# Performance work log

Hardware: AMD Instinct MI355X
Metric: run time of the kernel (lower is better)

Reference implementation:

```python
import jax, jax.numpy as jnp
import numpy as np

N = 100000      # nodes
E = 1600000     # edges (avg degree 16)
EMB = 128
L = 3           # num_layers
NUM_OPS = 64
MAX_BW = 64     # max_bitwidth
P = 4           # max_num_params


def setup_inputs() -> dict:
    key = jax.random.key(0)
    ks = jax.random.split(key, 24)
    w = lambda k, s: jax.random.normal(k, s, jnp.float32) * 0.05
    return {
        "ops": jax.random.randint(ks[0], (N,), 0, NUM_OPS),
        "params": jax.random.randint(ks[1], (N, P), 0, MAX_BW),
        "edge_src": jax.random.randint(ks[2], (E,), 0, N),
        "edge_dst": jax.random.randint(ks[3], (E,), 0, N),
        "op_emb_table": w(ks[4], (NUM_OPS, EMB)),
        "param_emb_table": w(ks[5], (MAX_BW, EMB)),
        "opmlp_w1": w(ks[6], ((1 + P) * EMB, EMB)), "opmlp_b1": w(ks[7], (EMB,)),
        "opmlp_w2": w(ks[8], (EMB, EMB)), "opmlp_b2": w(ks[9], (EMB,)),
        "conv_w": w(ks[10], (L, EMB, EMB)), "conv_b": w(ks[11], (L, EMB)),
        "mlp_w1": w(ks[12], (L * EMB, EMB)), "mlp_b1": w(ks[13], (EMB,)),
        "mlp_w2": w(ks[14], (EMB, EMB)), "mlp_b2": w(ks[15], (EMB,)),
        "mlpinv_w1": w(ks[16], (L * EMB, EMB)), "mlpinv_b1": w(ks[17], (EMB,)),
        "mlpinv_w2": w(ks[18], (EMB, EMB)), "mlpinv_b2": w(ks[19], (EMB,)),
        "comb_w": w(ks[20], (2 * EMB, EMB)), "comb_b": w(ks[21], (EMB,)),
    }


def _lrelu(x):
    return jax.nn.leaky_relu(x)  # slope 0.01, matches nn.LeakyReLU default


def _gin_mean(feat, src, dst, w, b):
    # DGL GINConv(aggregator='mean', eps=0): apply_func(feat + mean_in_neighbors(feat))
    n = feat.shape[0]
    msg = jax.ops.segment_sum(feat[src], dst, num_segments=n)           # [N, EMB]
    deg = jax.ops.segment_sum(jnp.ones(src.shape, feat.dtype), dst, num_segments=n)
    agg = msg / jnp.maximum(deg, 1.0)[:, None]
    return _lrelu((feat + agg) @ w + b)


def reference(ops, params, edge_src, edge_dst,
              op_emb_table, param_emb_table,
              opmlp_w1, opmlp_b1, opmlp_w2, opmlp_b2,
              conv_w, conv_b,
              mlp_w1, mlp_b1, mlp_w2, mlp_b2,
              mlpinv_w1, mlpinv_b1, mlpinv_w2, mlpinv_b2,
              comb_w, comb_b):
    n = ops.shape[0]
    # OpEmb: cat([op_emb] + per-param embs) -> MLP
    op_e = op_emb_table[ops]                               # [N, EMB]
    par_e = param_emb_table[params].reshape(n, -1)         # [N, P*EMB]
    h = jnp.concatenate([op_e, par_e], axis=1)
    h = _lrelu(h @ opmlp_w1 + opmlp_b1) @ opmlp_w2 + opmlp_b2
    states = h
    states_inv = h  # op_emb called twice on same inputs in the original

    conv_outs = []
    for i in range(L):
        states = _gin_mean(states, edge_src, edge_dst, conv_w[i], conv_b[i])
        conv_outs.append(states.sum(axis=0))
    final_sum = states.sum(axis=0)

    conv_outs_inv = []
    for i in range(L):
        states_inv = _gin_mean(states_inv, edge_dst, edge_src, conv_w[i], conv_b[i])
        # NOTE: original code appends states.sum(dim=0) (the final forward states),
        # not states_inv -- faithfully reproduced.
        conv_outs_inv.append(final_sum)

    g_emb = _lrelu(jnp.concatenate(conv_outs) @ mlp_w1 + mlp_b1) @ mlp_w2 + mlp_b2
    g_inv_emb = _lrelu(jnp.concatenate(conv_outs_inv) @ mlpinv_w1 + mlpinv_b1) @ mlpinv_w2 + mlpinv_b2

    out1 = jnp.concatenate([g_emb, g_inv_emb]) @ comb_w + comb_b          # [EMB]
    out2 = jnp.concatenate([states, states_inv], axis=1) @ comb_w + comb_b  # [N, EMB]
    return (out1, out2)
```

## Files before the change

### kernel.cpp

```cpp
#include <hip/hip_runtime.h>


typedef unsigned int  uint;
typedef unsigned short ushort;
typedef float  f32x4  __attribute__((ext_vector_type(4)));
typedef short  bf16x8 __attribute__((ext_vector_type(8)));

#define ABITS 9
#define CAPB  12288
#define CHUNK 2048

__device__ __forceinline__ float lrelu(float x) { return x > 0.0f ? x : 0.01f * x; }
__device__ __forceinline__ ushort f2b(float x) {
    uint u = __float_as_uint(x);
    return (ushort)((u + 0x7fffu + ((u >> 16) & 1u)) >> 16);
}
__device__ __forceinline__ float lof(uint u) { return __uint_as_float(u << 16); }
__device__ __forceinline__ float hif(uint u) { return __uint_as_float(u & 0xffff0000u); }

__global__ __launch_bounds__(256) void buildprep_kernel(
    const int* __restrict__ esrc, const int* __restrict__ edst, int E, int nb, int nChunks,
    int* __restrict__ gcur, uint2* __restrict__ binbuf,
    const float* __restrict__ opT, const float* __restrict__ parT,
    const float* __restrict__ W1, float* __restrict__ Atab,
    const float* __restrict__ convw, const float* __restrict__ ow2,
    const float* __restrict__ cw, ushort* __restrict__ Wt)
{
    __shared__ int hist[448];
    __shared__ int lstart[448];
    __shared__ int gbase[448];
    __shared__ int lcur[448];
    __shared__ int gsum[8];
    __shared__ uint sKey[CHUNK * 2];
    __shared__ uint sPay[CHUNK * 2];
    __shared__ ushort sBin[CHUNK * 2];
    int tid = threadIdx.x, lane = tid & 63;

    if ((int)blockIdx.x >= nChunks) {
        int rb = (int)blockIdx.x - nChunks;
        if (rb < 160) {
            int b = (rb << 1) | (tid >> 7);
            int t = b >> 6, v = b & 63, j = tid & 127;
            const float* emb = (t == 0 ? opT : parT) + v * 128;
            const float* w = W1 + (size_t)t * 128 * 128;
            float acc = 0.f;
            for (int k = 0; k < 128; ++k) acc += emb[k] * w[k * 128 + j];
            Atab[(size_t)b * 128 + j] = acc;
        } else {
            int t = (rb - 160) * 256 + tid;
            int img = t >> 14, idx = t & 16383;
            int k = idx >> 7, c = idx & 127;
            const float* src;
            if (img < 3)       src = convw + img * 16384;
            else if (img == 3) src = ow2;
            else               src = cw + (img - 4) * 16384;
            float v = src[k * 128 + c];
            int byteoff = (img << 15) + (c << 8) + ((((k >> 3) ^ (c & 7)) << 4)) + ((k & 7) << 1);
            Wt[byteoff >> 1] = f2b(v);
        }
        return;
    }

    int nb2 = nb * 2;
    int base = (int)blockIdx.x * CHUNK;
    int cnt = min(CHUNK, E - base);
    for (int i = tid; i < 448; i += 256) hist[i] = 0;
    __syncthreads();
    int s[8], d[8];
    #pragma unroll
    for (int i = 0; i < 8; ++i) {
        int idx = i * 256 + tid;
        if (idx < cnt) {
            s[i] = esrc[base + idx];
            d[i] = edst[base + idx];
            atomicAdd(&hist[d[i] >> ABITS], 1);
            atomicAdd(&hist[nb + (s[i] >> ABITS)], 1);
        } else s[i] = -1;
    }
    __syncthreads();
    #pragma unroll
    for (int k = 0; k < 2; ++k) {
        int idx = k * 256 + tid;
        int v = (idx < 448) ? hist[idx] : 0;
        int p = v;
        #pragma unroll
        for (int sh = 1; sh < 64; sh <<= 1) { int t = __shfl_up(p, sh, 64); if (lane >= sh) p += t; }
        if (idx < 448) {
            lstart[idx] = p - v;
            if (lane == 63) gsum[idx >> 6] = p;
        }
    }
    __syncthreads();
    if (tid == 0) { int run = 0; for (int g = 0; g < 7; ++g) { int t = gsum[g]; gsum[g] = run; run += t; } }
    __syncthreads();
    #pragma unroll
    for (int k = 0; k < 2; ++k) {
        int idx = k * 256 + tid;
        if (idx < 448) lstart[idx] += gsum[idx >> 6];
    }
    __syncthreads();
    for (int i = tid; i < nb2; i += 256) {
        int h = hist[i];
        gbase[i] = h ? atomicAdd(&gcur[i], h) : 0;
        lcur[i] = lstart[i];
    }
    __syncthreads();
    #pragma unroll
    for (int i = 0; i < 8; ++i) {
        if (s[i] >= 0) {
            int bf = d[i] >> ABITS;
            int p = atomicAdd(&lcur[bf], 1);
            sKey[p] = (uint)d[i]; sPay[p] = (uint)s[i]; sBin[p] = (ushort)bf;
            int bi = nb + (s[i] >> ABITS);
            int q = atomicAdd(&lcur[bi], 1);
            sKey[q] = (uint)s[i]; sPay[q] = (uint)d[i]; sBin[q] = (ushort)bi;
        }
    }
    __syncthreads();
    int total = 2 * cnt;
    for (int p = tid; p < total; p += 256) {
        int b = sBin[p];
        int pos = gbase[b] + (p - lstart[b]);
        if (pos < CAPB) binbuf[(size_t)b * CAPB + pos] = make_uint2(sKey[p], sPay[p]);
    }
}

__device__ __forceinline__ void stage_w(const ushort* __restrict__ img, ushort* ldsW, int tid)
{
    const uint4* s = (const uint4*)img;
    uint4* d = (uint4*)ldsW;
    #pragma unroll
    for (int i = 0; i < 4; ++i) d[tid + (i << 9)] = s[tid + (i << 9)];
}

__global__ __launch_bounds__(512, 2) void mid_kernel(
    const uint2* __restrict__ binbuf, const int* __restrict__ gcur, int nb, int N,
    int* __restrict__ csr_f, int* __restrict__ off_f, int* __restrict__ cnt_f,
    int* __restrict__ csr_i, int* __restrict__ off_i, int* __restrict__ cnt_i,
    const int* __restrict__ ops, const int* __restrict__ params,
    const float* __restrict__ Atab, const float* __restrict__ b1,
    const ushort* __restrict__ W2img, const float* __restrict__ b2,
    ushort* __restrict__ S0)
{
    __shared__ __align__(16) ushort ldsW[16384];
    __shared__ __align__(16) ushort ldsA[16384];
    int tid = threadIdx.x, lane = tid & 63, w = tid >> 6;
    int nb2 = 2 * nb;

    if ((int)blockIdx.x < nb2) {
        int* hist = (int*)ldsA;
        int* cur  = hist + 512;
        int* gsum = cur + 512;
        int b = blockIdx.x;
        int dir = (b >= nb) ? 1 : 0;
        int binLocal = dir ? b - nb : b;
        int node0 = binLocal << ABITS;
        int nn = min(512, N - node0);
        int total = min(gcur[b], CAPB);
        const uint2* seg = binbuf + (size_t)b * CAPB;
        int* csr = dir ? csr_i : csr_f;
        int* off = dir ? off_i : off_f;
        int* cnt = dir ? cnt_i : cnt_f;

        hist[tid] = 0;
        __syncthreads();
        for (int e = tid; e < total; e += 512) {
            uint2 kp = seg[e];
            atomicAdd(&hist[kp.x - (uint)node0], 1);
        }
        __syncthreads();
        int v = hist[tid];
        int p = v;
        #pragma unroll
        for (int sh = 1; sh < 64; sh <<= 1) { int t = __shfl_up(p, sh, 64); if (lane >= sh) p += t; }
        if (lane == 63) gsum[w] = p;
        __syncthreads();
        if (tid == 0) { int run = 0; for (int g = 0; g < 8; ++g) { int t = gsum[g]; gsum[g] = run; run += t; } }
        __syncthreads();
        int lv = p - v + gsum[w];
        cur[tid] = lv;
        int csrBase = binLocal * CAPB;
        if (tid < nn) { off[node0 + tid] = csrBase + lv; cnt[node0 + tid] = v; }
        __syncthreads();
        int* csrSeg = csr + csrBase;
        for (int e = tid; e < total; e += 512) {
            uint2 kp = seg[e];
            int q = atomicAdd(&cur[kp.x - (uint)node0], 1);
            csrSeg[q] = (int)(kp.y << 8);
        }
        return;
    }

    int node0 = ((int)blockIdx.x - nb2) << 7;
    stage_w(W2img, ldsW, tid);

    int r = tid >> 2, sub = tid & 3;
    int g = node0 + r;
    float4 acc4[8];
    if (g < N) {
        int op = ops[g];
        const float4* T = (const float4*)(Atab + ((size_t)op << 7) + (sub << 5));
        #pragma unroll
        for (int q = 0; q < 8; ++q) acc4[q] = T[q];
        #pragma unroll
        for (int p = 0; p < 4; ++p) {
            int pv = params[(g << 2) + p];
            const float4* Tp = (const float4*)(Atab + ((size_t)((p + 1) * 64 + pv) << 7) + (sub << 5));
            #pragma unroll
            for (int q = 0; q < 8; ++q) {
                float4 u = Tp[q];
                acc4[q].x += u.x; acc4[q].y += u.y; acc4[q].z += u.z; acc4[q].w += u.w;
            }
        }
        const float4* Bv = (const float4*)(b1 + (sub << 5));
        #pragma unroll
        for (int q = 0; q < 8; ++q) {
            float4 bb = Bv[q];
            acc4[q].x = lrelu(acc4[q].x + bb.x);
            acc4[q].y = lrelu(acc4[q].y + bb.y);
            acc4[q].z = lrelu(acc4[q].z + bb.z);
            acc4[q].w = lrelu(acc4[q].w + bb.w);
        }
    } else {
        #pragma unroll
        for (int q = 0; q < 8; ++q) acc4[q] = make_float4(0.f, 0.f, 0.f, 0.f);
    }
    int akey = r & 7;
    #pragma unroll
    for (int q2 = 0; q2 < 4; ++q2) {
        int ch = (sub << 2) + q2;
        float4 a = acc4[q2 * 2], b = acc4[q2 * 2 + 1];
        uint4 pk;
        pk.x = (uint)f2b(a.x) | ((uint)f2b(a.y) << 16);
        pk.y = (uint)f2b(a.z) | ((uint)f2b(a.w) << 16);
        pk.z = (uint)f2b(b.x) | ((uint)f2b(b.y) << 16);
        pk.w = (uint)f2b(b.z) | ((uint)f2b(b.w) << 16);
        *(uint4*)((char*)ldsA + r * 256 + ((ch ^ akey) << 4)) = pk;
    }
    __syncthreads();

    int l15 = lane & 15, lg = lane >> 4;
    int node = node0 + (w << 4) + l15;
    int brow = (w << 4) + l15;
    const char* Bb = (const char*)ldsA + brow * 256;
    int bkey = (brow & 7) << 4;
    f32x4 acc[8];
    #pragma unroll
    for (int i = 0; i < 8; ++i) acc[i] = f32x4{0.f, 0.f, 0.f, 0.f};
    #pragma unroll
    for (int kk = 0; kk < 4; ++kk) {
        bf16x8 bfr = *(const bf16x8*)(Bb + ((((kk << 2) + lg) << 4) ^ bkey));
        #pragma unroll
        for (int ct = 0; ct < 8; ++ct) {
            int c = (ct << 4) + l15;
            const char* Ab = (const char*)ldsW + c * 256;
            bf16x8 af = *(const bf16x8*)(Ab + ((((kk << 2) + lg) << 4) ^ ((c & 7) << 4)));
            acc[ct] = __builtin_amdgcn_mfma_f32_16x16x32_bf16(af, bfr, acc[ct], 0, 0, 0);
        }
    }
    if (node < N) {
        #pragma unroll
        for (int ct = 0; ct < 8; ++ct) {
            int ch0 = (ct << 4) + (lg << 2);
            float4 bb = *(const float4*)(b2 + ch0);
            uint2 pk;
            pk.x = (uint)f2b(acc[ct][0] + bb.x) | ((uint)f2b(acc[ct][1] + bb.y) << 16);
            pk.y = (uint)f2b(acc[ct][2] + bb.z) | ((uint)f2b(acc[ct][3] + bb.w) << 16);
            *(uint2*)((char*)S0 + ((size_t)node << 8) + (ch0 << 1)) = pk;
        }
    }
}

__global__ __launch_bounds__(256, 8) void agg2_kernel(
    const ushort* __restrict__ Sf, const ushort* __restrict__ Si,
    const int* __restrict__ csr_f, const int* __restrict__ off_f, const int* __restrict__ cnt_f,
    const int* __restrict__ csr_i, const int* __restrict__ off_i, const int* __restrict__ cnt_i,
    ushort* __restrict__ msgf, ushort* __restrict__ msgi, int N)
{
    int gw = (blockIdx.x * 256 + threadIdx.x) >> 6;
    int lane = threadIdx.x & 63;
    int dir = 0, g = gw;
    if (g >= N) { dir = 1; g -= N; if (g >= N) return; }
    const char* Sp = (const char*)(dir ? Si : Sf);
    const int* csr = dir ? csr_i : csr_f;
    int off = (dir ? off_i : off_f)[g];
    int deg = (dir ? cnt_i : cnt_f)[g];
    int half = lane >> 5;
    int lb = (lane & 31) << 3;

    float a0 = 0.f, a1 = 0.f, a2 = 0.f, a3 = 0.f;
    int d = 0;
    for (; d + 8 <= deg; d += 8) {
        int b0 = csr[off + d + 0 + half];
        int b1 = csr[off + d + 2 + half];
        int b2 = csr[off + d + 4 + half];
        int b3 = csr[off + d + 6 + half];
        uint2 v0 = *(const uint2*)(Sp + (uint)(b0 + lb));
        uint2 v1 = *(const uint2*)(Sp + (uint)(b1 + lb));
        uint2 v2 = *(const uint2*)(Sp + (uint)(b2 + lb));
        uint2 v3 = *(const uint2*)(Sp + (uint)(b3 + lb));
        a0 += (lof(v0.x) + lof(v1.x)) + (lof(v2.x) + lof(v3.x));
        a1 += (hif(v0.x) + hif(v1.x)) + (hif(v2.x) + hif(v3.x));
        a2 += (lof(v0.y) + lof(v1.y)) + (lof(v2.y) + lof(v3.y));
        a3 += (hif(v0.y) + hif(v1.y)) + (hif(v2.y) + hif(v3.y));
    }
    for (; d + 2 <= deg; d += 2) {
        int b = csr[off + d + half];
        uint2 v = *(const uint2*)(Sp + (uint)(b + lb));
        a0 += lof(v.x); a1 += hif(v.x); a2 += lof(v.y); a3 += hif(v.y);
    }
    if (d < deg && half == 0) {
        int b = csr[off + d];
        uint2 v = *(const uint2*)(Sp + (uint)(b + lb));
        a0 += lof(v.x); a1 += hif(v.x); a2 += lof(v.y); a3 += hif(v.y);
    }
    a0 += __shfl_xor(a0, 32);
    a1 += __shfl_xor(a1, 32);
    a2 += __shfl_xor(a2, 32);
    a3 += __shfl_xor(a3, 32);
    float invd = 1.0f / fmaxf((float)deg, 1.0f);
    uint2 self = *(const uint2*)(Sp + ((size_t)g << 8) + lb);
    a0 = lof(self.x) + a0 * invd;
    a1 = hif(self.x) + a1 * invd;
    a2 = lof(self.y) + a2 * invd;
    a3 = hif(self.y) + a3 * invd;
    if (half == 0) {
        uint2 pk;
        pk.x = (uint)f2b(a0) | ((uint)f2b(a1) << 16);
        pk.y = (uint)f2b(a2) | ((uint)f2b(a3) << 16);
        *(uint2*)((char*)(dir ? msgi : msgf) + ((size_t)g << 8) + lb) = pk;
    }
}

__global__ __launch_bounds__(512, 8) void gemm2_kernel(
    const ushort* __restrict__ msgf, const ushort* __restrict__ msgi,
    ushort* __restrict__ Sf_out, ushort* __restrict__ Si_out,
    const ushort* __restrict__ Wimg, const float* __restrict__ bias,
    float* __restrict__ colsum, int N)
{
    __shared__ __align__(16) ushort ldsW[16384];
    __shared__ float ldsCS[128];
    int tid = threadIdx.x, lane = tid & 63, w = tid >> 6;
    bool fwd = (blockIdx.x & 1) == 0;
    int node0 = (blockIdx.x >> 1) << 7;
    const ushort* msg = fwd ? msgf : msgi;
    ushort* Sout = fwd ? Sf_out : Si_out;

    stage_w(Wimg, ldsW, tid);
    if (fwd && tid < 128) ldsCS[tid] = 0.f;
    __syncthreads();

    int l15 = lane & 15, lg = lane >> 4;
    int node = node0 + (w << 4) + l15;
    int gr = min(node, N - 1);
    const char* Bb = (const char*)msg + ((size_t)gr << 8);

    f32x4 acc[8];
    #pragma unroll
    for (int i = 0; i < 8; ++i) acc[i] = f32x4{0.f, 0.f, 0.f, 0.f};
    #pragma unroll
    for (int kk = 0; kk < 4; ++kk) {
        bf16x8 bfr = *(const bf16x8*)(Bb + (((kk << 2) + lg) << 4));
        #pragma unroll
        for (int ct = 0; ct < 8; ++ct) {
            int c = (ct << 4) + l15;
            const char* Ab = (const char*)ldsW + c * 256;
            bf16x8 af = *(const bf16x8*)(Ab + ((((kk << 2) + lg) << 4) ^ ((c & 7) << 4)));
            acc[ct] = __builtin_amdgcn_mfma_f32_16x16x32_bf16(af, bfr, acc[ct], 0, 0, 0);
        }
    }

    bool valid = node < N;
    #pragma unroll
    for (int ct = 0; ct < 8; ++ct) {
        int ch0 = (ct << 4) + (lg << 2);
        float4 bb = *(const float4*)(bias + ch0);
        float o0 = lrelu(acc[ct][0] + bb.x);
        float o1 = lrelu(acc[ct][1] + bb.y);
        float o2 = lrelu(acc[ct][2] + bb.z);
        float o3 = lrelu(acc[ct][3] + bb.w);
        if (valid) {
            uint2 pk;
            pk.x = (uint)f2b(o0) | ((uint)f2b(o1) << 16);
            pk.y = (uint)f2b(o2) | ((uint)f2b(o3) << 16);
            *(uint2*)((char*)Sout + ((size_t)node << 8) + (ch0 << 1)) = pk;
        }
        if (fwd) {
            float c0 = valid ? o0 : 0.f, c1 = valid ? o1 : 0.f;
            float c2 = valid ? o2 : 0.f, c3 = valid ? o3 : 0.f;
            #pragma unroll
            for (int m = 1; m < 16; m <<= 1) {
                c0 += __shfl_xor(c0, m);
                c1 += __shfl_xor(c1, m);
                c2 += __shfl_xor(c2, m);
                c3 += __shfl_xor(c3, m);
            }
            if (l15 == 0) {
                atomicAdd(&ldsCS[ch0 + 0], c0);
                atomicAdd(&ldsCS[ch0 + 1], c1);
                atomicAdd(&ldsCS[ch0 + 2], c2);
                atomicAdd(&ldsCS[ch0 + 3], c3);
            }
        }
    }
    if (fwd) {
        __syncthreads();
        if (tid < 128) atomicAdd(&colsum[tid], ldsCS[tid]);
    }
}

__device__ __forceinline__ void final_body(
    float* lds, const float* __restrict__ convsum,
    const float* __restrict__ mw1, const float* __restrict__ mb1,
    const float* __restrict__ mw2, const float* __restrict__ mb2,
    const float* __restrict__ iw1, const float* __restrict__ ib1,
    const float* __restrict__ iw2, const float* __restrict__ ib2,
    const float* __restrict__ cw, const float* __restrict__ cb,
    float* __restrict__ out1)
{
    float* x  = lds;
    float* pa = lds + 384;
    float* pb = lds + 896;
    float* t1 = lds + 1408;
    float* t2 = lds + 1536;
    int tid = threadIdx.x, j = tid & 127, s = tid >> 7;
    if (tid < 384) x[tid] = convsum[tid];
    __syncthreads();
    float a = 0.f, c = 0.f;
    for (int k = s * 96; k < s * 96 + 96; ++k) {
        a += x[k] * mw1[k * 128 + j];
        c += x[256 + (k & 127)] * iw1[k * 128 + j];
    }
    pa[tid] = a; pb[tid] = c;
    __syncthreads();
    if (s == 0) {
        t1[j] = lrelu(pa[j] + pa[128 + j] + pa[256 + j] + pa[384 + j] + mb1[j]);
        t2[j] = lrelu(pb[j] + pb[128 + j] + pb[256 + j] + pb[384 + j] + ib1[j]);
    }
    __syncthreads();
    float b = 0.f, d = 0.f;
    for (int k = s * 32; k < s * 32 + 32; ++k) {
        b += t1[k] * mw2[k * 128 + j];
        d += t2[k] * iw2[k * 128 + j];
    }
    pa[tid] = b; pb[tid] = d;
    __syncthreads();
    if (s == 0) {
        t1[j] = pa[j] + pa[128 + j] + pa[256 + j] + pa[384 + j] + mb2[j];
        t2[j] = pb[j] + pb[128 + j] + pb[256 + j] + pb[384 + j] + ib2[j];
    }
    __syncthreads();
    float e = 0.f;
    for (int k = s * 32; k < s * 32 + 32; ++k)
        e += t1[k] * cw[k * 128 + j] + t2[k] * cw[(128 + k) * 128 + j];
    pa[tid] = e;
    __syncthreads();
    if (s == 0) out1[j] = pa[j] + pa[128 + j] + pa[256 + j] + pa[384 + j] + cb[j];
}

__global__ __launch_bounds__(512, 4) void out2_fused(
    const ushort* __restrict__ Sf, const ushort* __restrict__ Si,
    const ushort* __restrict__ CWimg, const float* __restrict__ cb,
    float* __restrict__ out, int gemmBlocks, int N,
    const float* __restrict__ convsum,
    const float* __restrict__ mw1, const float* __restrict__ mb1,
    const float* __restrict__ mw2, const float* __restrict__ mb2,
    const float* __restrict__ iw1, const float* __restrict__ ib1,
    const float* __restrict__ iw2, const float* __restrict__ ib2,
    const float* __restrict__ cw, float* __restrict__ out1)
{
    __shared__ __align__(16) ushort ldsW[16384];
    int tid = threadIdx.x, lane = tid & 63, w = tid >> 6;
    if ((int)blockIdx.x >= gemmBlocks) {
        final_body((float*)ldsW, convsum, mw1, mb1, mw2, mb2,
                   iw1, ib1, iw2, ib2, cw, cb, out1);
        return;
    }
    int node0 = blockIdx.x << 7;
    int l15 = lane & 15, lg = lane >> 4;
    int node = node0 + (w << 4) + l15;
    int gr = min(node, N - 1);
    f32x4 acc[8];
    #pragma unroll
    for (int i = 0; i < 8; ++i) acc[i] = f32x4{0.f, 0.f, 0.f, 0.f};
    #pragma unroll
    for (int pass = 0; pass < 2; ++pass) {
        if (pass) __syncthreads();
        stage_w(CWimg + (pass << 14), ldsW, tid);
        __syncthreads();
        const char* Bb = (const char*)(pass ? Si : Sf) + ((size_t)gr << 8);
        #pragma unroll
        for (int kk = 0; kk < 4; ++kk) {
            bf16x8 bfr = *(const bf16x8*)(Bb + (((kk << 2) + lg) << 4));
            #pragma unroll
            for (int ct = 0; ct < 8; ++ct) {
                int c = (ct << 4) + l15;
                const char* Ab = (const char*)ldsW + c * 256;
                bf16x8 af = *(const bf16x8*)(Ab + ((((kk << 2) + lg) << 4) ^ ((c & 7) << 4)));
                acc[ct] = __builtin_amdgcn_mfma_f32_16x16x32_bf16(af, bfr, acc[ct], 0, 0, 0);
            }
        }
    }
    if (node < N) {
        #pragma unroll
        for (int ct = 0; ct < 8; ++ct) {
            int ch0 = (ct << 4) + (lg << 2);
            float4 bb = *(const float4*)(cb + ch0);
            float4 o;
            o.x = acc[ct][0] + bb.x;
            o.y = acc[ct][1] + bb.y;
            o.z = acc[ct][2] + bb.z;
            o.w = acc[ct][3] + bb.w;
            *(float4*)(out + (size_t)node * 128 + ch0) = o;
        }
    }
}

extern "C" void kernel_launch(void* const* d_in, const int* in_sizes, int n_in,
                              void* d_out, int out_size, void* d_ws, size_t ws_size,
                              hipStream_t stream)
{
    (void)n_in; (void)out_size; (void)ws_size;
    const int*   ops    = (const int*)d_in[0];
    const int*   params = (const int*)d_in[1];
    const int*   esrc   = (const int*)d_in[2];
    const int*   edst   = (const int*)d_in[3];
    const float* opT    = (const float*)d_in[4];
    const float* parT   = (const float*)d_in[5];
    const float* ow1    = (const float*)d_in[6];
    const float* ob1    = (const float*)d_in[7];
    const float* ow2    = (const float*)d_in[8];
    const float* ob2    = (const float*)d_in[9];
    const float* convw  = (const float*)d_in[10];
    const float* convb  = (const float*)d_in[11];
    const float* mw1    = (const float*)d_in[12];
    const float* mb1    = (const float*)d_in[13];
    const float* mw2    = (const float*)d_in[14];
    const float* mb2    = (const float*)d_in[15];
    const float* iw1    = (const float*)d_in[16];
    const float* ib1    = (const float*)d_in[17];
    const float* iw2    = (const float*)d_in[18];
    const float* ib2    = (const float*)d_in[19];
    const float* cw     = (const float*)d_in[20];
    const float* cb     = (const float*)d_in[21];

    const int N = in_sizes[0];
    const int E = in_sizes[2];
    const int nb = (N + 511) >> ABITS;
    const size_t NP = (size_t)N * 128;

    ushort* S0   = (ushort*)d_ws;
    ushort* S1   = S0 + NP;
    ushort* S2   = S1 + NP;
    ushort* S3   = S2 + NP;
    ushort* Wt   = S3 + NP;
    float*  Atab = (float*)(Wt + 6 * 16384);
    float*  convsum = Atab + 320 * 128;
    int*    gcur = (int*)(convsum + 512);
    uint2*  binbuf = (uint2*)(gcur + 512);
    int*    csr_f = (int*)(binbuf + (size_t)2 * nb * CAPB);
    int*    csr_i = csr_f + (size_t)nb * CAPB;
    int*    off_f = csr_i + (size_t)nb * CAPB;
    int*    cnt_f = off_f + N;
    int*    off_i = cnt_f + N;
    int*    cnt_i = off_i + N;

    float* out1 = (float*)d_out;
    float* out2 = out1 + 128;
    ushort* MSGF = (ushort*)out2;
    ushort* MSGI = MSGF + NP;

    hipMemsetAsync(convsum, 0, sizeof(float) * 1024, stream);

    const int nChunks = (E + CHUNK - 1) / CHUNK;
    buildprep_kernel<<<nChunks + 160 + 384, 256, 0, stream>>>(
        esrc, edst, E, nb, nChunks, gcur, binbuf,
        opT, parT, ow1, Atab, convw, ow2, cw, Wt);

    const int grid = (N + 127) / 128;
    mid_kernel<<<2 * nb + grid, 512, 0, stream>>>(
        binbuf, gcur, nb, N,
        csr_f, off_f, cnt_f, csr_i, off_i, cnt_i,
        ops, params, Atab, ob1, Wt + 3 * 16384, ob2, S0);

    const int aggGrid = (2 * N + 3) / 4;
    agg2_kernel<<<aggGrid, 256, 0, stream>>>(S0, S0, csr_f, off_f, cnt_f, csr_i, off_i, cnt_i, MSGF, MSGI, N);
    gemm2_kernel<<<2 * grid, 512, 0, stream>>>(MSGF, MSGI, S1, S3, Wt,             convb,       convsum,       N);
    agg2_kernel<<<aggGrid, 256, 0, stream>>>(S1, S3, csr_f, off_f, cnt_f, csr_i, off_i, cnt_i, MSGF, MSGI, N);
    gemm2_kernel<<<2 * grid, 512, 0, stream>>>(MSGF, MSGI, S0, S2, Wt + 16384,     convb + 128, convsum + 128, N);
    agg2_kernel<<<aggGrid, 256, 0, stream>>>(S0, S2, csr_f, off_f, cnt_f, csr_i, off_i, cnt_i, MSGF, MSGI, N);
    gemm2_kernel<<<2 * grid, 512, 0, stream>>>(MSGF, MSGI, S1, S3, Wt + 2 * 16384, convb + 256, convsum + 256, N);

    out2_fused<<<grid + 1, 512, 0, stream>>>(S1, S3, Wt + 4 * 16384, cb, out2, grid, N,
                                             convsum, mw1, mb1, mw2, mb2,
                                             iw1, ib1, iw2, ib2, cw, out1);
}
```

Baseline: 655.3 us.

## Fuse GIN aggregation and layer GEMM into one kernel per layer

Merges the separate aggregation and GEMM kernels into one kernel per layer. Each 256-thread block gathers 16 nodes' mean-aggregated features into shared memory, then runs MFMA against weights read straight from global memory (no LDS staging). This drops the global round trip of the message buffers and three launches. Column-sum atomics are spread over 8 replicas, which the final kernel reduces. The cost is weight fragments fetched from global/L2 by every small block, and lower GEMM reuse per block.

```diff
diff --git a/kernel.cpp b/kernel.cpp
--- a/kernel.cpp
+++ b/kernel.cpp
@@ -271,141 +271,140 @@
     }
 }
 
-__global__ __launch_bounds__(256, 8) void agg2_kernel(
-    const ushort* __restrict__ Sf, const ushort* __restrict__ Si,
+__global__ __launch_bounds__(256, 8) void glayer_kernel(
+    const ushort* __restrict__ Sf_in, const ushort* __restrict__ Si_in,
+    ushort* __restrict__ Sf_out, ushort* __restrict__ Si_out,
     const int* __restrict__ csr_f, const int* __restrict__ off_f, const int* __restrict__ cnt_f,
     const int* __restrict__ csr_i, const int* __restrict__ off_i, const int* __restrict__ cnt_i,
-    ushort* __restrict__ msgf, ushort* __restrict__ msgi, int N)
+    const ushort* __restrict__ Wimg, const float* __restrict__ bias,
+    float* __restrict__ colsumR, int nBlkF, int N)
 {
-    int gw = (blockIdx.x * 256 + threadIdx.x) >> 6;
-    int lane = threadIdx.x & 63;
-    int dir = 0, g = gw;
-    if (g >= N) { dir = 1; g -= N; if (g >= N) return; }
-    const char* Sp = (const char*)(dir ? Si : Sf);
-    const int* csr = dir ? csr_i : csr_f;
-    int off = (dir ? off_i : off_f)[g];
-    int deg = (dir ? cnt_i : cnt_f)[g];
+    __shared__ __align__(16) char msgL[16 * 272];
+    __shared__ float ldsCS[128];
+    int tid = threadIdx.x, lane = tid & 63, w = tid >> 6;
+    bool fwd = (int)blockIdx.x < nBlkF;
+    int blkLocal = fwd ? (int)blockIdx.x : (int)blockIdx.x - nBlkF;
+    const char* Sp = (const char*)(fwd ? Sf_in : Si_in);
+    ushort* Sout = fwd ? Sf_out : Si_out;
+    const int* csr  = fwd ? csr_f : csr_i;
+    const int* offA = fwd ? off_f : off_i;
+    const int* cntA = fwd ? cnt_f : cnt_i;
+
+    if (tid < 128) ldsCS[tid] = 0.f;
+
     int half = lane >> 5;
     int lb = (lane & 31) << 3;
-
-    float a0 = 0.f, a1 = 0.f, a2 = 0.f, a3 = 0.f;
-    int d = 0;
-    for (; d + 8 <= deg; d += 8) {
-        int b0 = csr[off + d + 0 + half];
-        int b1 = csr[off + d + 2 + half];
-        int b2 = csr[off + d + 4 + half];
-        int b3 = csr[off + d + 6 + half];
-        uint2 v0 = *(const uint2*)(Sp + (uint)(b0 + lb));
-        uint2 v1 = *(const uint2*)(Sp + (uint)(b1 + lb));
-        uint2 v2 = *(const uint2*)(Sp + (uint)(b2 + lb));
-        uint2 v3 = *(const uint2*)(Sp + (uint)(b3 + lb));
-        a0 += (lof(v0.x) + lof(v1.x)) + (lof(v2.x) + lof(v3.x));
-        a1 += (hif(v0.x) + hif(v1.x)) + (hif(v2.x) + hif(v3.x));
-        a2 += (lof(v0.y) + lof(v1.y)) + (lof(v2.y) + lof(v3.y));
-        a3 += (hif(v0.y) + hif(v1.y)) + (hif(v2.y) + hif(v3.y));
-    }
-    for (; d + 2 <= deg; d += 2) {
-        int b = csr[off + d + half];
-        uint2 v = *(const uint2*)(Sp + (uint)(b + lb));
-        a0 += lof(v.x); a1 += hif(v.x); a2 += lof(v.y); a3 += hif(v.y);
-    }
-    if (d < deg && half == 0) {
-        int b = csr[off + d];
-        uint2 v = *(const uint2*)(Sp + (uint)(b + lb));
-        a0 += lof(v.x); a1 += hif(v.x); a2 += lof(v.y); a3 += hif(v.y);
-    }
-    a0 += __shfl_xor(a0, 32);
-    a1 += __shfl_xor(a1, 32);
-    a2 += __shfl_xor(a2, 32);
-    a3 += __shfl_xor(a3, 32);
-    float invd = 1.0f / fmaxf((float)deg, 1.0f);
-    uint2 self = *(const uint2*)(Sp + ((size_t)g << 8) + lb);
-    a0 = lof(self.x) + a0 * invd;
-    a1 = hif(self.x) + a1 * invd;
-    a2 = lof(self.y) + a2 * invd;
-    a3 = hif(self.y) + a3 * invd;
-    if (half == 0) {
-        uint2 pk;
-        pk.x = (uint)f2b(a0) | ((uint)f2b(a1) << 16);
-        pk.y = (uint)f2b(a2) | ((uint)f2b(a3) << 16);
-        *(uint2*)((char*)(dir ? msgi : msgf) + ((size_t)g << 8) + lb) = pk;
-    }
-}
-
-__global__ __launch_bounds__(512, 8) void gemm2_kernel(
-    const ushort* __restrict__ msgf, const ushort* __restrict__ msgi,
-    ushort* __restrict__ Sf_out, ushort* __restrict__ Si_out,
-    const ushort* __restrict__ Wimg, const float* __restrict__ bias,
-    float* __restrict__ colsum, int N)
-{
-    __shared__ __align__(16) ushort ldsW[16384];
-    __shared__ float ldsCS[128];
-    int tid = threadIdx.x, lane = tid & 63, w = tid >> 6;
-    bool fwd = (blockIdx.x & 1) == 0;
-    int node0 = (blockIdx.x >> 1) << 7;
-    const ushort* msg = fwd ? msgf : msgi;
-    ushort* Sout = fwd ? Sf_out : Si_out;
-
-    stage_w(Wimg, ldsW, tid);
-    if (fwd && tid < 128) ldsCS[tid] = 0.f;
+    int node0 = blkLocal << 4;
+
+    #pragma unroll
+    for (int i = 0; i < 4; ++i) {
+        int g = node0 + (w << 2) + i;
+        float a0 = 0.f, a1 = 0.f, a2 = 0.f, a3 = 0.f;
+        if (g < N) {
+            int off = offA[g], deg = cntA[g];
+            int d = 0;
+            for (; d + 8 <= deg; d += 8) {
+                int b0 = csr[off + d + 0 + half];
+                int b1 = csr[off + d + 2 + half];
+                int b2 = csr[off + d + 4 + half];
+                int b3 = csr[off + d + 6 + half];
+                uint2 v0 = *(const uint2*)(Sp + (uint)(b0 + lb));
+                uint2 v1 = *(const uint2*)(Sp + (uint)(b1 + lb));
+                uint2 v2 = *(const uint2*)(Sp + (uint)(b2 + lb));
+                uint2 v3 = *(const uint2*)(Sp + (uint)(b3 + lb));
+                a0 += (lof(v0.x) + lof(v1.x)) + (lof(v2.x) + lof(v3.x));
+                a1 += (hif(v0.x) + hif(v1.x)) + (hif(v2.x) + hif(v3.x));
+                a2 += (lof(v0.y) + lof(v1.y)) + (lof(v2.y) + lof(v3.y));
+                a3 += (hif(v0.y) + hif(v1.y)) + (hif(v2.y) + hif(v3.y));
+            }
+            for (; d + 2 <= deg; d += 2) {
+                int b = csr[off + d + half];
+                uint2 v = *(const uint2*)(Sp + (uint)(b + lb));
+                a0 += lof(v.x); a1 += hif(v.x); a2 += lof(v.y); a3 += hif(v.y);
+            }
+            if (d < deg && half == 0) {
+                int b = csr[off + d];
+                uint2 v = *(const uint2*)(Sp + (uint)(b + lb));
+                a0 += lof(v.x); a1 += hif(v.x); a2 += lof(v.y); a3 += hif(v.y);
+            }
+            a0 += __shfl_xor(a0, 32);
+            a1 += __shfl_xor(a1, 32);
+            a2 += __shfl_xor(a2, 32);
+            a3 += __shfl_xor(a3, 32);
+            float iv = 1.0f / fmaxf((float)deg, 1.0f);
+            uint2 self = *(const uint2*)(Sp + ((size_t)g << 8) + lb);
+            a0 = lof(self.x) + a0 * iv;
+            a1 = hif(self.x) + a1 * iv;
+            a2 = lof(self.y) + a2 * iv;
+            a3 = hif(self.y) + a3 * iv;
+        }
+        if (half == 0) {
+            uint2 pk;
+            pk.x = (uint)f2b(a0) | ((uint)f2b(a1) << 16);
+            pk.y = (uint)f2b(a2) | ((uint)f2b(a3) << 16);
+            *(uint2*)(msgL + ((w << 2) + i) * 272 + lb) = pk;
+        }
+    }
     __syncthreads();
 
     int l15 = lane & 15, lg = lane >> 4;
-    int node = node0 + (w << 4) + l15;
-    int gr = min(node, N - 1);
-    const char* Bb = (const char*)msg + ((size_t)gr << 8);
-
-    f32x4 acc[8];
-    #pragma unroll
-    for (int i = 0; i < 8; ++i) acc[i] = f32x4{0.f, 0.f, 0.f, 0.f};
+    const char* Bb = msgL + l15 * 272;
+    f32x4 acc0 = f32x4{0.f, 0.f, 0.f, 0.f};
+    f32x4 acc1 = f32x4{0.f, 0.f, 0.f, 0.f};
+    int ct0 = w << 1;
+    int c0 = (ct0 << 4) + l15;
+    int c1 = ((ct0 + 1) << 4) + l15;
+    const char* A0 = (const char*)Wimg + c0 * 256;
+    const char* A1 = (const char*)Wimg + c1 * 256;
+    int k0 = (c0 & 7) << 4, k1 = (c1 & 7) << 4;
     #pragma unroll
     for (int kk = 0; kk < 4; ++kk) {
-        bf16x8 bfr = *(const bf16x8*)(Bb + (((kk << 2) + lg) << 4));
-        #pragma unroll
-        for (int ct = 0; ct < 8; ++ct) {
-            int c = (ct << 4) + l15;
-            const char* Ab = (const char*)ldsW + c * 256;
-            bf16x8 af = *(const bf16x8*)(Ab + ((((kk << 2) + lg) << 4) ^ ((c & 7) << 4)));
-            acc[ct] = __builtin_amdgcn_mfma_f32_16x16x32_bf16(af, bfr, acc[ct], 0, 0, 0);
-        }
-    }
-
-    bool valid = node < N;
-    #pragma unroll
-    for (int ct = 0; ct < 8; ++ct) {
-        int ch0 = (ct << 4) + (lg << 2);
+        int chk = ((kk << 2) + lg) << 4;
+        bf16x8 bfr = *(const bf16x8*)(Bb + chk);
+        bf16x8 af0 = *(const bf16x8*)(A0 + (chk ^ k0));
+        bf16x8 af1 = *(const bf16x8*)(A1 + (chk ^ k1));
+        acc0 = __builtin_amdgcn_mfma_f32_16x16x32_bf16(af0, bfr, acc0, 0, 0, 0);
+        acc1 = __builtin_amdgcn_mfma_f32_16x16x32_bf16(af1, bfr, acc1, 0, 0, 0);
+    }
+
+    int gs = node0 + l15;
+    bool valid = gs < N;
+    #pragma unroll
+    for (int q = 0; q < 2; ++q) {
+        f32x4 a = q ? acc1 : acc0;
+        int ch0 = ((ct0 + q) << 4) + (lg << 2);
         float4 bb = *(const float4*)(bias + ch0);
-        float o0 = lrelu(acc[ct][0] + bb.x);
-        float o1 = lrelu(acc[ct][1] + bb.y);
-        float o2 = lrelu(acc[ct][2] + bb.z);
-        float o3 = lrelu(acc[ct][3] + bb.w);
+        float o0 = lrelu(a[0] + bb.x);
+        float o1 = lrelu(a[1] + bb.y);
+        float o2 = lrelu(a[2] + bb.z);
+        float o3 = lrelu(a[3] + bb.w);
         if (valid) {
             uint2 pk;
             pk.x = (uint)f2b(o0) | ((uint)f2b(o1) << 16);
             pk.y = (uint)f2b(o2) | ((uint)f2b(o3) << 16);
-            *(uint2*)((char*)Sout + ((size_t)node << 8) + (ch0 << 1)) = pk;
+            *(uint2*)((char*)Sout + ((size_t)gs << 8) + (ch0 << 1)) = pk;
         }
         if (fwd) {
-            float c0 = valid ? o0 : 0.f, c1 = valid ? o1 : 0.f;
-            float c2 = valid ? o2 : 0.f, c3 = valid ? o3 : 0.f;
+            float s0 = valid ? o0 : 0.f, s1 = valid ? o1 : 0.f;
+            float s2 = valid ? o2 : 0.f, s3 = valid ? o3 : 0.f;
             #pragma unroll
             for (int m = 1; m < 16; m <<= 1) {
-                c0 += __shfl_xor(c0, m);
-                c1 += __shfl_xor(c1, m);
-                c2 += __shfl_xor(c2, m);
-                c3 += __shfl_xor(c3, m);
+                s0 += __shfl_xor(s0, m);
+                s1 += __shfl_xor(s1, m);
+                s2 += __shfl_xor(s2, m);
+                s3 += __shfl_xor(s3, m);
             }
             if (l15 == 0) {
-                atomicAdd(&ldsCS[ch0 + 0], c0);
-                atomicAdd(&ldsCS[ch0 + 1], c1);
-                atomicAdd(&ldsCS[ch0 + 2], c2);
-                atomicAdd(&ldsCS[ch0 + 3], c3);
+                atomicAdd(&ldsCS[ch0 + 0], s0);
+                atomicAdd(&ldsCS[ch0 + 1], s1);
+                atomicAdd(&ldsCS[ch0 + 2], s2);
+                atomicAdd(&ldsCS[ch0 + 3], s3);
             }
         }
     }
     if (fwd) {
         __syncthreads();
-        if (tid < 128) atomicAdd(&colsum[tid], ldsCS[tid]);
+        if (tid < 128) atomicAdd(&colsumR[(((int)blockIdx.x & 7) << 7) + tid], ldsCS[tid]);
     }
 }
 
@@ -424,7 +423,13 @@
     float* t1 = lds + 1408;
     float* t2 = lds + 1536;
     int tid = threadIdx.x, j = tid & 127, s = tid >> 7;
-    if (tid < 384) x[tid] = convsum[tid];
+    if (tid < 384) {
+        const float* cs = convsum + (((size_t)(tid >> 7)) << 10) + (tid & 127);
+        float acc = 0.f;
+        #pragma unroll
+        for (int r = 0; r < 8; ++r) acc += cs[r << 7];
+        x[tid] = acc;
+    }
     __syncthreads();
     float a = 0.f, c = 0.f;
     for (int k = s * 96; k < s * 96 + 96; ++k) {
@@ -556,7 +561,7 @@
     ushort* Wt   = S3 + NP;
     float*  Atab = (float*)(Wt + 6 * 16384);
     float*  convsum = Atab + 320 * 128;
-    int*    gcur = (int*)(convsum + 512);
+    int*    gcur = (int*)(convsum + 3072);
     uint2*  binbuf = (uint2*)(gcur + 512);
     int*    csr_f = (int*)(binbuf + (size_t)2 * nb * CAPB);
     int*    csr_i = csr_f + (size_t)nb * CAPB;
@@ -567,10 +572,8 @@
 
     float* out1 = (float*)d_out;
     float* out2 = out1 + 128;
-    ushort* MSGF = (ushort*)out2;
-    ushort* MSGI = MSGF + NP;
-
-    hipMemsetAsync(convsum, 0, sizeof(float) * 1024, stream);
+
+    hipMemsetAsync(convsum, 0, sizeof(float) * 3584, stream);
 
     const int nChunks = (E + CHUNK - 1) / CHUNK;
     buildprep_kernel<<<nChunks + 160 + 384, 256, 0, stream>>>(
@@ -583,13 +586,16 @@
         csr_f, off_f, cnt_f, csr_i, off_i, cnt_i,
         ops, params, Atab, ob1, Wt + 3 * 16384, ob2, S0);
 
-    const int aggGrid = (2 * N + 3) / 4;
-    agg2_kernel<<<aggGrid, 256, 0, stream>>>(S0, S0, csr_f, off_f, cnt_f, csr_i, off_i, cnt_i, MSGF, MSGI, N);
-    gemm2_kernel<<<2 * grid, 512, 0, stream>>>(MSGF, MSGI, S1, S3, Wt,             convb,       convsum,       N);
-    agg2_kernel<<<aggGrid, 256, 0, stream>>>(S1, S3, csr_f, off_f, cnt_f, csr_i, off_i, cnt_i, MSGF, MSGI, N);
-    gemm2_kernel<<<2 * grid, 512, 0, stream>>>(MSGF, MSGI, S0, S2, Wt + 16384,     convb + 128, convsum + 128, N);
-    agg2_kernel<<<aggGrid, 256, 0, stream>>>(S0, S2, csr_f, off_f, cnt_f, csr_i, off_i, cnt_i, MSGF, MSGI, N);
-    gemm2_kernel<<<2 * grid, 512, 0, stream>>>(MSGF, MSGI, S1, S3, Wt + 2 * 16384, convb + 256, convsum + 256, N);
+    const int nBlkF = (N + 15) / 16;
+    glayer_kernel<<<2 * nBlkF, 256, 0, stream>>>(S0, S0, S1, S3,
+        csr_f, off_f, cnt_f, csr_i, off_i, cnt_i,
+        Wt,             convb,       convsum,        nBlkF, N);
+    glayer_kernel<<<2 * nBlkF, 256, 0, stream>>>(S1, S3, S0, S2,
+        csr_f, off_f, cnt_f, csr_i, off_i, cnt_i,
+        Wt + 16384,     convb + 128, convsum + 1024, nBlkF, N);
+    glayer_kernel<<<2 * nBlkF, 256, 0, stream>>>(S0, S2, S1, S3,
+        csr_f, off_f, cnt_f, csr_i, off_i, cnt_i,
+        Wt + 2 * 16384, convb + 256, convsum + 2048, nBlkF, N);
 
     out2_fused<<<grid + 1, 512, 0, stream>>>(S1, S3, Wt + 4 * 16384, cb, out2, grid, N,
                                              convsum, mw1, mb1, mw2, mb2,
```

Measured after the change: 599.5 us. -8.5%, faster.
